# Kernel optimization log

Measured on AMD Instinct MI355X. Metric: run time of the kernel, lower is better.

Reference implementation:

```python
import jax, jax.numpy as jnp
import numpy as np

N_DFT = 512
N_FILTER = N_DFT // 2 + 1  # 257
N_HOP = N_DFT // 2         # 256
AMIN = 1e-10
DYNAMIC_RANGE = 80.0


def _dft_kernels(n_dft):
    """Windowed real-DFT kernels, shape (n_dft, n_filter) each."""
    n_filter = n_dft // 2 + 1
    n = np.arange(n_dft)
    # periodic Hann (scipy.signal.hann(n_dft, sym=False))
    win = 0.5 - 0.5 * np.cos(2.0 * np.pi * n / n_dft)
    ang = 2.0 * np.pi * np.outer(n, np.arange(n_filter)) / n_dft  # (n_dft, n_filter)
    k_real = (np.cos(ang) * win[:, None]).astype(np.float32)
    k_imag = (np.sin(ang) * win[:, None]).astype(np.float32)
    return jnp.asarray(k_real), jnp.asarray(k_imag)


def setup_inputs() -> dict:
    key = jax.random.key(0)
    x = jax.random.normal(key, (32, 2, 262144), dtype=jnp.float32)  # (batch, ch, samples)
    k_real, k_imag = _dft_kernels(N_DFT)
    return {"x": x, "k_real": k_real, "k_imag": k_imag}


def reference(x, k_real, k_imag):
    n_dft = k_real.shape[0]
    n_hop = n_dft // 2
    B, C, L = x.shape
    # TF/Keras 'same' padding with stride n_hop
    n_frame = -(-L // n_hop)
    rem = L % n_hop
    pad_total = max(n_dft - n_hop, 0) if rem == 0 else max(n_dft - rem, 0)
    pad_l = pad_total // 2
    xp = jnp.pad(x, ((0, 0), (0, 0), (pad_l, pad_total - pad_l)))
    # frame the signal: (B, C, n_frame, n_dft)
    idx = jnp.arange(n_frame)[:, None] * n_hop + jnp.arange(n_dft)[None, :]
    frames = xp[:, :, idx]
    # DFT via dense GEMM with cos/sin kernels
    re = jnp.einsum('bctd,df->bctf', frames, k_real)
    im = jnp.einsum('bctd,df->bctf', frames, k_imag)
    power = re * re + im * im  # (B, C, n_frame, n_filter)
    # channels_last output: (B, n_freq, n_time, n_ch)
    out = jnp.transpose(power, (0, 3, 2, 1))
    # power_spectrogram == 2.0 -> no pow adjustment; decibel conversion:
    log10 = jnp.float32(np.log(10.0))
    log_spec = 10.0 * jnp.log(jnp.maximum(out, AMIN)) / log10
    log_spec = log_spec - jnp.max(log_spec)
    return jnp.maximum(log_spec, -DYNAMIC_RANGE)
```

## Files before the change

kernel.cpp:

```cpp
#include <hip/hip_runtime.h>
#include <math.h>

#define L_IN     262144
#define N_FRAME  1024
#define AMIN     1e-10f
#define DRANGE   80.0f
#define UNITS_CH 1056
#define WS_HI_OFF   4096
#define WS_HALF     524288
#define N4_OUT   ((32 * 257 * 1024 * 2) / 4)

typedef short bf16x8 __attribute__((ext_vector_type(8)));
typedef short bf16x4 __attribute__((ext_vector_type(4)));
typedef float f32x16 __attribute__((ext_vector_type(16)));

__device__ __forceinline__ short f2bf(float f) {
    unsigned u = __float_as_uint(f);
    u = (u + 0x7FFFu + ((u >> 16) & 1u)) >> 16;
    return (short)u;
}
__device__ __forceinline__ float bf2f(short h) {
    return __uint_as_float(((unsigned)(unsigned short)h) << 16);
}
__device__ __forceinline__ int swz(int u) { return u ^ ((u >> 5) & 7); }

__global__ __launch_bounds__(256) void wconv_kernel(
    const float* __restrict__ kr, const float* __restrict__ ki,
    short* __restrict__ whi, short* __restrict__ wlo, unsigned* __restrict__ wsmax)
{
    if (blockIdx.x == 0 && threadIdx.x == 0) wsmax[0] = 0u;
    const int tid  = threadIdx.x;
    const int pair = blockIdx.x * 4 + (tid >> 6);
    const int lane = tid & 63;
    const int fi = pair >> 5, kk = pair & 31;
    const int g = fi >> 1, nf = fi & 1;
    const int n  = lane & 31;
    const int k0 = kk * 16 + (lane >> 5) * 8;
    const int f  = g * 32 + n;
    bf16x8 h8, l8;
    #pragma unroll
    for (int j = 0; j < 8; ++j) {
        const int k = k0 + j;
        float w;
        if (nf == 1 && g == 0 && n == 0) w = kr[k * 257 + 256];
        else                             w = (nf ? ki : kr)[k * 257 + f];
        short hh = f2bf(w);
        h8[j] = hh;
        l8[j] = f2bf(w - bf2f(hh));
    }
    const int off = ((fi * 32 + kk) * 64 + lane) * 8;
    *(bf16x8*)(whi + off) = h8;
    *(bf16x8*)(wlo + off) = l8;
}

__global__ __launch_bounds__(512) void spec_kernel(
    const float* __restrict__ x,
    const short* __restrict__ whi, const short* __restrict__ wlo,
    float* __restrict__ out, unsigned* __restrict__ wsmax)
{
    __shared__ __align__(16) char smem[2 * 2 * UNITS_CH * 8 * sizeof(short)];
    __shared__ float wmax[8];
    short* Ah = (short*)smem;
    short* Al = (short*)(smem + 2 * UNITS_CH * 8 * sizeof(short));
    float* S  = (float*)smem;

    const int blk = blockIdx.x;
    const int tt  = blk & 31;
    const int b   = blk >> 5;
    const int tid = threadIdx.x;
    const int lane = tid & 63;
    const int g    = tid >> 6;
    const int col  = lane & 31;
    const int half = lane >> 5;

    const int s_origin = tt * 8192 - 128;
    for (int cc = g; cc < 66; cc += 8) {
        const int ch   = (cc >= 33) ? 1 : 0;
        const int c    = cc - ch * 33;
        const int base = s_origin + c * 256;
        const float* xp = x + ((size_t)b * 2 + ch) * L_IN;
        const int i4 = base + lane * 4;
        float v[4];
        if (base >= 0 && base + 256 <= L_IN) {
            float4 p = *(const float4*)(xp + i4);
            v[0] = p.x; v[1] = p.y; v[2] = p.z; v[3] = p.w;
        } else {
            #pragma unroll
            for (int j = 0; j < 4; ++j) {
                const int idx = i4 + j;
                v[j] = (idx >= 0 && idx < L_IN) ? xp[idx] : 0.0f;
            }
        }
        bf16x4 h4, l4;
        #pragma unroll
        for (int j = 0; j < 4; ++j) {
            short hh = f2bf(v[j]);
            h4[j] = hh;
            l4[j] = f2bf(v[j] - bf2f(hh));
        }
        const int u = c * 32 + (lane >> 1);
        const int e = (ch * UNITS_CH + swz(u)) * 8 + (lane & 1) * 4;
        *(bf16x4*)&Ah[e] = h4;
        *(bf16x4*)&Al[e] = l4;
    }
    __syncthreads();

    f32x16 acc[2][2];
    #pragma unroll
    for (int mf = 0; mf < 2; ++mf)
        #pragma unroll
        for (int nf = 0; nf < 2; ++nf)
            #pragma unroll
            for (int r = 0; r < 16; ++r) acc[mf][nf][r] = 0.0f;

    const int laneoff = lane * 8;
    bf16x8 bh[2][2], bl[2][2];
    #pragma unroll
    for (int nf = 0; nf < 2; ++nf)
        #pragma unroll
        for (int kh = 0; kh < 2; ++kh) {
            const int off = (((g * 2 + nf) * 32 + kh) * 64) * 8 + laneoff;
            bh[nf][kh] = *(const bf16x8*)(whi + off);
            bl[nf][kh] = *(const bf16x8*)(wlo + off);
        }

    for (int kp = 0; kp < 16; ++kp) {
        bf16x8 ah[2][2], al[2][2];
        #pragma unroll
        for (int mf = 0; mf < 2; ++mf)
            #pragma unroll
            for (int kh = 0; kh < 2; ++kh) {
                const int u = col * 32 + kp * 4 + kh * 2 + half;
                const int e = (mf * UNITS_CH + swz(u)) * 8;
                ah[mf][kh] = *(const bf16x8*)&Ah[e];
                al[mf][kh] = *(const bf16x8*)&Al[e];
            }
        bf16x8 nbh[2][2], nbl[2][2];
        if (kp < 15) {
            #pragma unroll
            for (int nf = 0; nf < 2; ++nf)
                #pragma unroll
                for (int kh = 0; kh < 2; ++kh) {
                    const int off = (((g * 2 + nf) * 32 + (kp + 1) * 2 + kh) * 64) * 8 + laneoff;
                    nbh[nf][kh] = *(const bf16x8*)(whi + off);
                    nbl[nf][kh] = *(const bf16x8*)(wlo + off);
                }
        }
        #pragma unroll
        for (int kh = 0; kh < 2; ++kh)
            #pragma unroll
            for (int mf = 0; mf < 2; ++mf)
                #pragma unroll
                for (int nf = 0; nf < 2; ++nf)
                    acc[mf][nf] = __builtin_amdgcn_mfma_f32_32x32x16_bf16(ah[mf][kh], bh[nf][kh], acc[mf][nf], 0, 0, 0);
        #pragma unroll
        for (int kh = 0; kh < 2; ++kh)
            #pragma unroll
            for (int mf = 0; mf < 2; ++mf)
                #pragma unroll
                for (int nf = 0; nf < 2; ++nf)
                    acc[mf][nf] = __builtin_amdgcn_mfma_f32_32x32x16_bf16(al[mf][kh], bh[nf][kh], acc[mf][nf], 0, 0, 0);
        #pragma unroll
        for (int kh = 0; kh < 2; ++kh)
            #pragma unroll
            for (int mf = 0; mf < 2; ++mf)
                #pragma unroll
                for (int nf = 0; nf < 2; ++nf)
                    acc[mf][nf] = __builtin_amdgcn_mfma_f32_32x32x16_bf16(ah[mf][kh], bl[nf][kh], acc[mf][nf], 0, 0, 0);
        #pragma unroll
        for (int nf = 0; nf < 2; ++nf)
            #pragma unroll
            for (int kh = 0; kh < 2; ++kh) {
                bh[nf][kh] = nbh[nf][kh]; bl[nf][kh] = nbl[nf][kh];
            }
    }

    __syncthreads();
    const bool nyq = (g == 0) && (col == 0);
    float pmax = 0.0f;
    #pragma unroll
    for (int mf = 0; mf < 2; ++mf) {
        #pragma unroll
        for (int r = 0; r < 16; ++r) {
            const int m = (r & 3) + 8 * (r >> 2) + 4 * half;
            const float re = acc[mf][0][r];
            const float im = acc[mf][1][r];
            const float imq = nyq ? 0.0f : im;
            float p = fmaxf(re * re + imq * imq, AMIN);
            pmax = fmaxf(pmax, p);
            S[(m * 2 + mf) * 257 + g * 32 + col] = p;
            if (nyq) {
                float pn = fmaxf(im * im, AMIN);
                pmax = fmaxf(pmax, pn);
                S[(m * 2 + mf) * 257 + 256] = pn;
            }
        }
    }
    #pragma unroll
    for (int off = 32; off > 0; off >>= 1)
        pmax = fmaxf(pmax, __shfl_down(pmax, off, 64));
    if (lane == 0) wmax[g] = pmax;
    __syncthreads();
    if (tid == 0) {
        float m2 = wmax[0];
        #pragma unroll
        for (int w = 1; w < 8; ++w) m2 = fmaxf(m2, wmax[w]);
        atomicMax(wsmax, __float_as_uint(m2));
    }
    float* obase = out + (size_t)b * 526336 + (size_t)tt * 64;
    for (int q = tid; q < 257 * 16; q += 512) {
        const int f = q >> 4, part = q & 15;
        float4 vv;
        vv.x = S[(part * 4 + 0) * 257 + f];
        vv.y = S[(part * 4 + 1) * 257 + f];
        vv.z = S[(part * 4 + 2) * 257 + f];
        vv.w = S[(part * 4 + 3) * 257 + f];
        *(float4*)(obase + (size_t)f * 2048 + part * 4) = vv;
    }
}

__global__ __launch_bounds__(256) void finalize_kernel(
    float* __restrict__ out, const unsigned* __restrict__ ws_max, int n4)
{
    const int i = blockIdx.x * 256 + threadIdx.x;
    if (i >= n4) return;
    const float mlog = 10.0f * log10f(__uint_as_float(*ws_max));
    float4 p = ((const float4*)out)[i];
    float4 v;
    v.x = fmaxf(10.0f * log10f(p.x) - mlog, -DRANGE);
    v.y = fmaxf(10.0f * log10f(p.y) - mlog, -DRANGE);
    v.z = fmaxf(10.0f * log10f(p.z) - mlog, -DRANGE);
    v.w = fmaxf(10.0f * log10f(p.w) - mlog, -DRANGE);
    ((float4*)out)[i] = v;
}

extern "C" void kernel_launch(void* const* d_in, const int* in_sizes, int n_in,
                              void* d_out, int out_size, void* d_ws, size_t ws_size,
                              hipStream_t stream) {
    const float* x  = (const float*)d_in[0];
    const float* kr = (const float*)d_in[1];
    const float* ki = (const float*)d_in[2];
    float* out      = (float*)d_out;

    unsigned* wsmax = (unsigned*)d_ws;
    short* whi      = (short*)((char*)d_ws + WS_HI_OFF);
    short* wlo      = (short*)((char*)d_ws + WS_HI_OFF + WS_HALF);

    wconv_kernel<<<128, 256, 0, stream>>>(kr, ki, whi, wlo, wsmax);

    const int nblocks = 32 * 32;
    spec_kernel<<<nblocks, 512, 0, stream>>>(x, whi, wlo, out, wsmax);

    const int n4 = N4_OUT;
    finalize_kernel<<<(n4 + 255) / 256, 256, 0, stream>>>(out, wsmax, n4);
}
```

Before: 224.1 us.

## Double frames per block to reuse DFT weight fragments across two M-subtiles

Each block now handles 64 frames per channel instead of 32, halving the grid. For every K step, each weight fragment loaded from global is applied to two accumulator sets, halving weight traffic per frame. Input loads are batched into registers before the bf16 split, and the output store becomes scalar per-element writes. The costs are more registers (launch_bounds 512,2 requested), a larger LDS tile, fewer blocks to fill the GPU, and less vectorised output stores.

New measurement: 215.5 us. 1.04x faster.

```diff
diff --git a/kernel.cpp b/kernel.cpp
--- a/kernel.cpp
+++ b/kernel.cpp
@@ -5,7 +5,7 @@
 #define N_FRAME  1024
 #define AMIN     1e-10f
 #define DRANGE   80.0f
-#define UNITS_CH 1056
+#define UNITS_CH 2080
 #define WS_HI_OFF   4096
 #define WS_HALF     524288
 #define N4_OUT   ((32 * 257 * 1024 * 2) / 4)
@@ -53,7 +53,7 @@
     *(bf16x8*)(wlo + off) = l8;
 }
 
-__global__ __launch_bounds__(512) void spec_kernel(
+__global__ __launch_bounds__(512, 2) void spec_kernel(
     const float* __restrict__ x,
     const short* __restrict__ whi, const short* __restrict__ wlo,
     float* __restrict__ out, unsigned* __restrict__ wsmax)
@@ -65,137 +65,161 @@
     float* S  = (float*)smem;
 
     const int blk = blockIdx.x;
-    const int tt  = blk & 31;
-    const int b   = blk >> 5;
+    const int tt  = blk & 15;
+    const int b   = blk >> 4;
     const int tid = threadIdx.x;
     const int lane = tid & 63;
     const int g    = tid >> 6;
     const int col  = lane & 31;
     const int half = lane >> 5;
 
-    const int s_origin = tt * 8192 - 128;
-    for (int cc = g; cc < 66; cc += 8) {
-        const int ch   = (cc >= 33) ? 1 : 0;
-        const int c    = cc - ch * 33;
-        const int base = s_origin + c * 256;
-        const float* xp = x + ((size_t)b * 2 + ch) * L_IN;
-        const int i4 = base + lane * 4;
-        float v[4];
-        if (base >= 0 && base + 256 <= L_IN) {
-            float4 p = *(const float4*)(xp + i4);
-            v[0] = p.x; v[1] = p.y; v[2] = p.z; v[3] = p.w;
-        } else {
+    const int s_origin = tt * 16384 - 128;
+    float4 pv[17];
+    #pragma unroll
+    for (int it = 0; it < 17; ++it) {
+        const int cc = g + it * 8;
+        if (cc < 130) {
+            const int ch   = (cc >= 65) ? 1 : 0;
+            const int c    = cc - ch * 65;
+            const int base = s_origin + c * 256;
+            const float* xp = x + ((size_t)b * 2 + ch) * L_IN;
+            const int i4 = base + lane * 4;
+            if (base >= 0 && base + 256 <= L_IN) {
+                pv[it] = *(const float4*)(xp + i4);
+            } else {
+                float4 t;
+                t.x = (i4     >= 0 && i4     < L_IN) ? xp[i4]     : 0.0f;
+                t.y = (i4 + 1 >= 0 && i4 + 1 < L_IN) ? xp[i4 + 1] : 0.0f;
+                t.z = (i4 + 2 >= 0 && i4 + 2 < L_IN) ? xp[i4 + 2] : 0.0f;
+                t.w = (i4 + 3 >= 0 && i4 + 3 < L_IN) ? xp[i4 + 3] : 0.0f;
+                pv[it] = t;
+            }
+        }
+    }
+    #pragma unroll
+    for (int it = 0; it < 17; ++it) {
+        const int cc = g + it * 8;
+        if (cc < 130) {
+            const int ch = (cc >= 65) ? 1 : 0;
+            const int c  = cc - ch * 65;
+            float v[4];
+            v[0] = pv[it].x; v[1] = pv[it].y; v[2] = pv[it].z; v[3] = pv[it].w;
+            bf16x4 h4, l4;
             #pragma unroll
             for (int j = 0; j < 4; ++j) {
-                const int idx = i4 + j;
-                v[j] = (idx >= 0 && idx < L_IN) ? xp[idx] : 0.0f;
-            }
-        }
-        bf16x4 h4, l4;
-        #pragma unroll
-        for (int j = 0; j < 4; ++j) {
-            short hh = f2bf(v[j]);
-            h4[j] = hh;
-            l4[j] = f2bf(v[j] - bf2f(hh));
-        }
-        const int u = c * 32 + (lane >> 1);
-        const int e = (ch * UNITS_CH + swz(u)) * 8 + (lane & 1) * 4;
-        *(bf16x4*)&Ah[e] = h4;
-        *(bf16x4*)&Al[e] = l4;
+                short hh = f2bf(v[j]);
+                h4[j] = hh;
+                l4[j] = f2bf(v[j] - bf2f(hh));
+            }
+            const int u = c * 32 + (lane >> 1);
+            const int e = (ch * UNITS_CH + swz(u)) * 8 + (lane & 1) * 4;
+            *(bf16x4*)&Ah[e] = h4;
+            *(bf16x4*)&Al[e] = l4;
+        }
     }
     __syncthreads();
 
-    f32x16 acc[2][2];
-    #pragma unroll
-    for (int mf = 0; mf < 2; ++mf)
-        #pragma unroll
-        for (int nf = 0; nf < 2; ++nf)
-            #pragma unroll
-            for (int r = 0; r < 16; ++r) acc[mf][nf][r] = 0.0f;
+    f32x16 acc[2][2][2];
+    #pragma unroll
+    for (int s = 0; s < 2; ++s)
+        #pragma unroll
+        for (int mf = 0; mf < 2; ++mf)
+            #pragma unroll
+            for (int nf = 0; nf < 2; ++nf)
+                #pragma unroll
+                for (int r = 0; r < 16; ++r) acc[s][mf][nf][r] = 0.0f;
 
     const int laneoff = lane * 8;
-    bf16x8 bh[2][2], bl[2][2];
+    bf16x8 bh[2][2];
     #pragma unroll
     for (int nf = 0; nf < 2; ++nf)
         #pragma unroll
-        for (int kh = 0; kh < 2; ++kh) {
-            const int off = (((g * 2 + nf) * 32 + kh) * 64) * 8 + laneoff;
-            bh[nf][kh] = *(const bf16x8*)(whi + off);
-            bl[nf][kh] = *(const bf16x8*)(wlo + off);
-        }
+        for (int kh = 0; kh < 2; ++kh)
+            bh[nf][kh] = *(const bf16x8*)(whi + (((g * 2 + nf) * 32 + kh) * 64) * 8 + laneoff);
 
     for (int kp = 0; kp < 16; ++kp) {
-        bf16x8 ah[2][2], al[2][2];
-        #pragma unroll
-        for (int mf = 0; mf < 2; ++mf)
-            #pragma unroll
-            for (int kh = 0; kh < 2; ++kh) {
-                const int u = col * 32 + kp * 4 + kh * 2 + half;
-                const int e = (mf * UNITS_CH + swz(u)) * 8;
-                ah[mf][kh] = *(const bf16x8*)&Ah[e];
-                al[mf][kh] = *(const bf16x8*)&Al[e];
-            }
-        bf16x8 nbh[2][2], nbl[2][2];
+        bf16x8 nbh[2][2], bl[2][2];
+        #pragma unroll
+        for (int s = 0; s < 2; ++s) {
+            bf16x8 ah[2][2], al[2][2];
+            #pragma unroll
+            for (int mf = 0; mf < 2; ++mf)
+                #pragma unroll
+                for (int kh = 0; kh < 2; ++kh) {
+                    const int u = s * 1024 + col * 32 + kp * 4 + kh * 2 + half;
+                    const int e = (mf * UNITS_CH + swz(u)) * 8;
+                    ah[mf][kh] = *(const bf16x8*)&Ah[e];
+                    al[mf][kh] = *(const bf16x8*)&Al[e];
+                }
+            if (s == 0) {
+                #pragma unroll
+                for (int nf = 0; nf < 2; ++nf)
+                    #pragma unroll
+                    for (int kh = 0; kh < 2; ++kh)
+                        bl[nf][kh] = *(const bf16x8*)(wlo + (((g * 2 + nf) * 32 + kp * 2 + kh) * 64) * 8 + laneoff);
+                if (kp < 15) {
+                    #pragma unroll
+                    for (int nf = 0; nf < 2; ++nf)
+                        #pragma unroll
+                        for (int kh = 0; kh < 2; ++kh)
+                            nbh[nf][kh] = *(const bf16x8*)(whi + (((g * 2 + nf) * 32 + (kp + 1) * 2 + kh) * 64) * 8 + laneoff);
+                }
+            }
+            #pragma unroll
+            for (int kh = 0; kh < 2; ++kh)
+                #pragma unroll
+                for (int mf = 0; mf < 2; ++mf)
+                    #pragma unroll
+                    for (int nf = 0; nf < 2; ++nf)
+                        acc[s][mf][nf] = __builtin_amdgcn_mfma_f32_32x32x16_bf16(ah[mf][kh], bh[nf][kh], acc[s][mf][nf], 0, 0, 0);
+            #pragma unroll
+            for (int kh = 0; kh < 2; ++kh)
+                #pragma unroll
+                for (int mf = 0; mf < 2; ++mf)
+                    #pragma unroll
+                    for (int nf = 0; nf < 2; ++nf)
+                        acc[s][mf][nf] = __builtin_amdgcn_mfma_f32_32x32x16_bf16(al[mf][kh], bh[nf][kh], acc[s][mf][nf], 0, 0, 0);
+            #pragma unroll
+            for (int kh = 0; kh < 2; ++kh)
+                #pragma unroll
+                for (int mf = 0; mf < 2; ++mf)
+                    #pragma unroll
+                    for (int nf = 0; nf < 2; ++nf)
+                        acc[s][mf][nf] = __builtin_amdgcn_mfma_f32_32x32x16_bf16(ah[mf][kh], bl[nf][kh], acc[s][mf][nf], 0, 0, 0);
+        }
         if (kp < 15) {
             #pragma unroll
             for (int nf = 0; nf < 2; ++nf)
                 #pragma unroll
-                for (int kh = 0; kh < 2; ++kh) {
-                    const int off = (((g * 2 + nf) * 32 + (kp + 1) * 2 + kh) * 64) * 8 + laneoff;
-                    nbh[nf][kh] = *(const bf16x8*)(whi + off);
-                    nbl[nf][kh] = *(const bf16x8*)(wlo + off);
-                }
-        }
-        #pragma unroll
-        for (int kh = 0; kh < 2; ++kh)
-            #pragma unroll
-            for (int mf = 0; mf < 2; ++mf)
-                #pragma unroll
-                for (int nf = 0; nf < 2; ++nf)
-                    acc[mf][nf] = __builtin_amdgcn_mfma_f32_32x32x16_bf16(ah[mf][kh], bh[nf][kh], acc[mf][nf], 0, 0, 0);
-        #pragma unroll
-        for (int kh = 0; kh < 2; ++kh)
-            #pragma unroll
-            for (int mf = 0; mf < 2; ++mf)
-                #pragma unroll
-                for (int nf = 0; nf < 2; ++nf)
-                    acc[mf][nf] = __builtin_amdgcn_mfma_f32_32x32x16_bf16(al[mf][kh], bh[nf][kh], acc[mf][nf], 0, 0, 0);
-        #pragma unroll
-        for (int kh = 0; kh < 2; ++kh)
-            #pragma unroll
-            for (int mf = 0; mf < 2; ++mf)
-                #pragma unroll
-                for (int nf = 0; nf < 2; ++nf)
-                    acc[mf][nf] = __builtin_amdgcn_mfma_f32_32x32x16_bf16(ah[mf][kh], bl[nf][kh], acc[mf][nf], 0, 0, 0);
-        #pragma unroll
-        for (int nf = 0; nf < 2; ++nf)
-            #pragma unroll
-            for (int kh = 0; kh < 2; ++kh) {
-                bh[nf][kh] = nbh[nf][kh]; bl[nf][kh] = nbl[nf][kh];
-            }
+                for (int kh = 0; kh < 2; ++kh)
+                    bh[nf][kh] = nbh[nf][kh];
+        }
     }
 
     __syncthreads();
     const bool nyq = (g == 0) && (col == 0);
     float pmax = 0.0f;
     #pragma unroll
-    for (int mf = 0; mf < 2; ++mf) {
-        #pragma unroll
-        for (int r = 0; r < 16; ++r) {
-            const int m = (r & 3) + 8 * (r >> 2) + 4 * half;
-            const float re = acc[mf][0][r];
-            const float im = acc[mf][1][r];
-            const float imq = nyq ? 0.0f : im;
-            float p = fmaxf(re * re + imq * imq, AMIN);
-            pmax = fmaxf(pmax, p);
-            S[(m * 2 + mf) * 257 + g * 32 + col] = p;
-            if (nyq) {
-                float pn = fmaxf(im * im, AMIN);
-                pmax = fmaxf(pmax, pn);
-                S[(m * 2 + mf) * 257 + 256] = pn;
-            }
-        }
-    }
+    for (int s = 0; s < 2; ++s)
+        #pragma unroll
+        for (int mf = 0; mf < 2; ++mf) {
+            #pragma unroll
+            for (int r = 0; r < 16; ++r) {
+                const int m   = (r & 3) + 8 * (r >> 2) + 4 * half;
+                const int row = (s * 32 + m) * 2 + mf;
+                const float re = acc[s][mf][0][r];
+                const float im = acc[s][mf][1][r];
+                const float imq = nyq ? 0.0f : im;
+                float p = fmaxf(re * re + imq * imq, AMIN);
+                pmax = fmaxf(pmax, p);
+                S[row * 257 + g * 32 + col] = p;
+                if (nyq) {
+                    float pn = fmaxf(im * im, AMIN);
+                    pmax = fmaxf(pmax, pn);
+                    S[row * 257 + 256] = pn;
+                }
+            }
+        }
     #pragma unroll
     for (int off = 32; off > 0; off >>= 1)
         pmax = fmaxf(pmax, __shfl_down(pmax, off, 64));
@@ -207,15 +231,10 @@
         for (int w = 1; w < 8; ++w) m2 = fmaxf(m2, wmax[w]);
         atomicMax(wsmax, __float_as_uint(m2));
     }
-    float* obase = out + (size_t)b * 526336 + (size_t)tt * 64;
-    for (int q = tid; q < 257 * 16; q += 512) {
-        const int f = q >> 4, part = q & 15;
-        float4 vv;
-        vv.x = S[(part * 4 + 0) * 257 + f];
-        vv.y = S[(part * 4 + 1) * 257 + f];
-        vv.z = S[(part * 4 + 2) * 257 + f];
-        vv.w = S[(part * 4 + 3) * 257 + f];
-        *(float4*)(obase + (size_t)f * 2048 + part * 4) = vv;
+    float* obase = out + (size_t)b * 526336 + (size_t)tt * 128;
+    for (int q = tid; q < 257 * 128; q += 512) {
+        const int f = q >> 7, tl2 = q & 127;
+        obase[(size_t)f * 2048 + tl2] = S[tl2 * 257 + f];
     }
 }
 
@@ -248,7 +267,7 @@
 
     wconv_kernel<<<128, 256, 0, stream>>>(kr, ki, whi, wlo, wsmax);
 
-    const int nblocks = 32 * 32;
+    const int nblocks = 32 * 16;
     spec_kernel<<<nblocks, 512, 0, stream>>>(x, whi, wlo, out, wsmax);
 
     const int n4 = N4_OUT;
```
